# Performance work log

Hardware: AMD Instinct MI355X
Metric: run time of the kernel (lower is better)

The kernel has to match this reference:

```python
import jax, jax.numpy as jnp
import numpy as np

NUM_HEADS = 8


def _rope(t):
    # t: (b, h, L, hd). Interleaved-pair rotary embedding (rotary_embedding_torch style).
    hd = t.shape[-1]
    L = t.shape[-2]
    inv_freq = 1.0 / (10000.0 ** (jnp.arange(0, hd, 2, dtype=jnp.float32) / hd))  # (hd/2,)
    freqs = jnp.arange(L, dtype=jnp.float32)[:, None] * inv_freq[None, :]          # (L, hd/2)
    cos = jnp.repeat(jnp.cos(freqs), 2, axis=-1)  # (L, hd) interleaved
    sin = jnp.repeat(jnp.sin(freqs), 2, axis=-1)
    x2 = t.reshape(t.shape[:-1] + (hd // 2, 2))
    rot = jnp.stack((-x2[..., 1], x2[..., 0]), axis=-1).reshape(t.shape)
    return t * cos + rot * sin


def setup_inputs() -> dict:
    key = jax.random.key(0)
    ks = jax.random.split(key, 6)
    b, L, d = 2, 2048, 512
    s = 1.0 / np.sqrt(d)
    return {
        "x": jax.random.normal(ks[0], (b, L, d), jnp.float32),
        "prev": jax.random.normal(ks[1], (b, NUM_HEADS, L, L), jnp.float32) * 0.1,
        "Wq": jax.random.normal(ks[2], (d, d), jnp.float32) * s,
        "bq": jnp.zeros((d,), jnp.float32),
        "Wk": jax.random.normal(ks[3], (d, d), jnp.float32) * s,
        "bk": jnp.zeros((d,), jnp.float32),
        "Wv": jax.random.normal(ks[4], (d, d), jnp.float32) * s,
        "bv": jnp.zeros((d,), jnp.float32),
    }


def reference(x, prev, Wq, bq, Wk, bk, Wv, bv):
    b, L, d = x.shape
    h = NUM_HEADS
    hd = d // h

    def proj(W, bias):
        # torch nn.Linear: y = x @ W.T + b, then split heads -> (b, h, L, hd)
        return (x @ W.T + bias).reshape(b, L, h, hd).transpose(0, 2, 1, 3)

    q = _rope(proj(Wq, bq))
    k = _rope(proj(Wk, bk))
    v = proj(Wv, bv)

    score = jnp.einsum('bhqd,bhkd->bhqk', q, k) / np.float32(np.sqrt(hd))
    causal = jnp.tril(jnp.ones((L, L), dtype=bool))
    score = jnp.where(causal[None, None], score, jnp.float32(-1e9))
    score = score + prev  # RealFormer-style residual attention bias
    attn = jax.nn.softmax(score, axis=-1)
    o = jnp.einsum('bhqk,bhkd->bhqd', attn, v).transpose(0, 2, 1, 3).reshape(b, L, d)
    return o, score
```

## Files before the change

### kernel.cpp

```cpp
#include <hip/hip_runtime.h>
#include <hip/hip_bf16.h>
#include <math.h>

#define L_SEQ 2048
#define DM 512
#define NH 8
#define HD 64
#define ROPE_C 0.4152410118609203f

typedef __attribute__((ext_vector_type(8))) short bf16x8;
typedef __attribute__((ext_vector_type(8))) unsigned short u16x8;
typedef __attribute__((ext_vector_type(4))) float f32x4;

#define MFMA16(a, b, c) __builtin_amdgcn_mfma_f32_16x16x32_bf16((a), (b), (c), 0, 0, 0)

static __device__ __forceinline__ unsigned short f2bf(float f) {
    union { float f; unsigned int u; } c; c.f = f;
    unsigned int r = (c.u + 0x7fffu + ((c.u >> 16) & 1u)) >> 16;
    return (unsigned short)r;
}
static __device__ __forceinline__ float bf2f(unsigned short h) {
    union { unsigned int u; float f; } c; c.u = ((unsigned int)h) << 16;
    return c.f;
}

__global__ __launch_bounds__(256) void qkv_proj_mfma(
    const float* __restrict__ x,
    const float* __restrict__ Wq, const float* __restrict__ bq,
    const float* __restrict__ Wk, const float* __restrict__ bk,
    const float* __restrict__ Wv, const float* __restrict__ bv,
    unsigned short* __restrict__ Qh, unsigned short* __restrict__ Ql,
    unsigned short* __restrict__ Kh, unsigned short* __restrict__ Kl,
    unsigned short* __restrict__ Vb)
{
    const int z = blockIdx.z;
    const float* __restrict__ W    = (z == 0) ? Wq : (z == 1) ? Wk : Wv;
    const float* __restrict__ bias = (z == 0) ? bq : (z == 1) ? bk : bv;

    __shared__ __align__(16) unsigned short Xh[64 * 64];
    __shared__ __align__(16) unsigned short Xl[64 * 64];
    __shared__ __align__(16) unsigned short Wh[64 * 64];
    __shared__ __align__(16) unsigned short Wl[64 * 64];

    const int t = threadIdx.x;
    const int w = t >> 6, l = t & 63;
    const int lr = l & 15, lg = l >> 4;
    const int mbase = blockIdx.x * 64;
    const int nbase = blockIdx.y * 64;

    const int sr = t & 63;
    const int sc = (t >> 6) * 16;

    f32x4 acc[4];
    #pragma unroll
    for (int nb = 0; nb < 4; ++nb) acc[nb] = (f32x4){0.f, 0.f, 0.f, 0.f};

    for (int k0 = 0; k0 < DM; k0 += 64) {
        __syncthreads();
        {
            const int ch0 = (t >> 6) * 2, sw = sr & 7;
            const float* xs = &x[(size_t)(mbase + sr) * DM + k0 + sc];
            const float* ws = &W[(size_t)(nbase + sr) * DM + k0 + sc];
            float xv[16], wv[16];
            #pragma unroll
            for (int i = 0; i < 4; ++i) {
                float4 a = *(const float4*)(xs + 4 * i);
                xv[4 * i + 0] = a.x; xv[4 * i + 1] = a.y; xv[4 * i + 2] = a.z; xv[4 * i + 3] = a.w;
                float4 b = *(const float4*)(ws + 4 * i);
                wv[4 * i + 0] = b.x; wv[4 * i + 1] = b.y; wv[4 * i + 2] = b.z; wv[4 * i + 3] = b.w;
            }
            u16x8 xh0, xl0, xh1, xl1, wh0, wl0, wh1, wl1;
            #pragma unroll
            for (int i = 0; i < 8; ++i) {
                unsigned short h;
                h = f2bf(xv[i]);     xh0[i] = h; xl0[i] = f2bf(xv[i] - bf2f(h));
                h = f2bf(xv[i + 8]); xh1[i] = h; xl1[i] = f2bf(xv[i + 8] - bf2f(h));
                h = f2bf(wv[i]);     wh0[i] = h; wl0[i] = f2bf(wv[i] - bf2f(h));
                h = f2bf(wv[i + 8]); wh1[i] = h; wl1[i] = f2bf(wv[i + 8] - bf2f(h));
            }
            *(u16x8*)&Xh[sr * 64 + (((ch0    ) ^ sw) << 3)] = xh0;
            *(u16x8*)&Xh[sr * 64 + (((ch0 + 1) ^ sw) << 3)] = xh1;
            *(u16x8*)&Xl[sr * 64 + (((ch0    ) ^ sw) << 3)] = xl0;
            *(u16x8*)&Xl[sr * 64 + (((ch0 + 1) ^ sw) << 3)] = xl1;
            *(u16x8*)&Wh[sr * 64 + (((ch0    ) ^ sw) << 3)] = wh0;
            *(u16x8*)&Wh[sr * 64 + (((ch0 + 1) ^ sw) << 3)] = wh1;
            *(u16x8*)&Wl[sr * 64 + (((ch0    ) ^ sw) << 3)] = wl0;
            *(u16x8*)&Wl[sr * 64 + (((ch0 + 1) ^ sw) << 3)] = wl1;
        }
        __syncthreads();

        #pragma unroll
        for (int kc = 0; kc < 2; ++kc) {
            const int arow = w * 16 + lr;
            const int aofs = arow * 64 + (((4 * kc + lg) ^ (arow & 7)) << 3);
            bf16x8 ah = *(const bf16x8*)&Xh[aofs];
            bf16x8 al = *(const bf16x8*)&Xl[aofs];
            #pragma unroll
            for (int nb = 0; nb < 4; ++nb) {
                const int brow = nb * 16 + lr;
                const int bofs = brow * 64 + (((4 * kc + lg) ^ (brow & 7)) << 3);
                bf16x8 bh_ = *(const bf16x8*)&Wh[bofs];
                bf16x8 bl_ = *(const bf16x8*)&Wl[bofs];
                acc[nb] = MFMA16(ah, bl_, acc[nb]);
                acc[nb] = MFMA16(al, bh_, acc[nb]);
                acc[nb] = MFMA16(ah, bh_, acc[nb]);
            }
        }
    }

    #pragma unroll
    for (int nb = 0; nb < 4; ++nb) {
        const int n    = nbase + nb * 16 + lr;
        const int head = n >> 6;
        const int dim  = n & 63;
        const float bval = bias[n];
        const float invf = exp2f(-ROPE_C * (float)(dim >> 1));
        #pragma unroll
        for (int r = 0; r < 4; ++r) {
            const int mg    = mbase + w * 16 + lg * 4 + r;
            const int batch = mg >> 11;
            const int pos   = mg & 2047;
            float v = acc[nb][r] + bval;
            if (z < 2) {
                const float pv = __shfl_xor(v, 1);
                float s, c;
                sincosf((float)pos * invf, &s, &c);
                v = (dim & 1) ? fmaf(v, c, pv * s) : fmaf(v, c, -pv * s);
            }
            const size_t oidx = (((size_t)(batch * NH + head)) * L_SEQ + pos) * HD + dim;
            if (z == 2) {
                Vb[oidx] = f2bf(v);
            } else {
                const unsigned short h  = f2bf(v);
                const unsigned short lo = f2bf(v - bf2f(h));
                if (z == 0) { Qh[oidx] = h; Ql[oidx] = lo; }
                else        { Kh[oidx] = h; Kl[oidx] = lo; }
            }
        }
    }
}

__global__ __launch_bounds__(256) void attn_mfma(
    const unsigned short* __restrict__ Qh, const unsigned short* __restrict__ Ql,
    const unsigned short* __restrict__ Kh, const unsigned short* __restrict__ Kl,
    const unsigned short* __restrict__ Vb, const float* __restrict__ prev,
    float* __restrict__ out_o, float* __restrict__ out_score)
{
    __shared__ __align__(16) unsigned short Ksh[64 * 64];
    __shared__ __align__(16) unsigned short Ksl[64 * 64];
    __shared__ __align__(16) unsigned short Vt[64 * 64];
    __shared__ __align__(16) unsigned short Ps[4 * 16 * 64];

    const int g  = blockIdx.x;
    const int bh = g & 15;
    const int gq = g >> 4;
    const int qt = (gq < 16) ? 31 - gq : gq - 16;
    const int t  = threadIdx.x;
    const int w  = t >> 6, l = t & 63;
    const int lr = l & 15, lg = l >> 4;
    const int qbase = qt << 6;

    const size_t hbase = (size_t)bh * L_SEQ * HD;

    bf16x8 qhf[2], qlf[2];
    {
        const size_t qoff = hbase + (size_t)(qbase + w * 16 + lr) * HD + lg * 8;
        qhf[0] = *(const bf16x8*)&Qh[qoff];
        qhf[1] = *(const bf16x8*)&Qh[qoff + 32];
        qlf[0] = *(const bf16x8*)&Ql[qoff];
        qlf[1] = *(const bf16x8*)&Ql[qoff + 32];
    }

    f32x4 accO[4];
    #pragma unroll
    for (int db = 0; db < 4; ++db) accO[db] = (f32x4){0.f, 0.f, 0.f, 0.f};
    float m_i[4] = {-INFINITY, -INFINITY, -INFINITY, -INFINITY};
    float l_i[4] = {0.f, 0.f, 0.f, 0.f};

    for (int kt = 0; kt <= qt; ++kt) {
        const int kbase = kt << 6;
        __syncthreads();

        const size_t srow = ((size_t)bh * L_SEQ + (qbase + w * 16)) * L_SEQ + kbase;
        float pvv[4][4];
        #pragma unroll
        for (int kb = 0; kb < 4; ++kb)
            #pragma unroll
            for (int r = 0; r < 4; ++r)
                pvv[kb][r] = prev[srow + (size_t)(lg * 4 + r) * L_SEQ + kb * 16 + lr];

        {
            const int r = t & 63, c32 = t >> 6;
            const int ch0 = 2 * c32, sw = r & 7;
            const size_t koff = hbase + (size_t)(kbase + r) * HD + c32 * 16;
            u16x8 k0 = *(const u16x8*)&Kh[koff];
            u16x8 k1 = *(const u16x8*)&Kh[koff + 8];
            *(u16x8*)&Ksh[r * 64 + (((ch0    ) ^ sw) << 3)] = k0;
            *(u16x8*)&Ksh[r * 64 + (((ch0 + 1) ^ sw) << 3)] = k1;
            u16x8 k2 = *(const u16x8*)&Kl[koff];
            u16x8 k3 = *(const u16x8*)&Kl[koff + 8];
            *(u16x8*)&Ksl[r * 64 + (((ch0    ) ^ sw) << 3)] = k2;
            *(u16x8*)&Ksl[r * 64 + (((ch0 + 1) ^ sw) << 3)] = k3;

            const int vk = t & 63, vd0 = (t >> 6) * 16;
            const size_t voff = hbase + (size_t)(kbase + vk) * HD + vd0;
            u16x8 va = *(const u16x8*)&Vb[voff];
            u16x8 vb2 = *(const u16x8*)&Vb[voff + 8];
            #pragma unroll
            for (int e = 0; e < 8; ++e) {
                int d = vd0 + e;
                Vt[d * 64 + ((((vk >> 3) ^ (d & 7))) << 3) + (vk & 7)] = va[e];
                d = vd0 + 8 + e;
                Vt[d * 64 + ((((vk >> 3) ^ (d & 7))) << 3) + (vk & 7)] = vb2[e];
            }
        }
        __syncthreads();

        f32x4 s[4];
        #pragma unroll
        for (int kb = 0; kb < 4; ++kb) s[kb] = (f32x4){0.f, 0.f, 0.f, 0.f};
        #pragma unroll
        for (int kc = 0; kc < 2; ++kc) {
            #pragma unroll
            for (int kb = 0; kb < 4; ++kb) {
                const int brow = kb * 16 + lr;
                const int bofs = brow * 64 + (((4 * kc + lg) ^ (brow & 7)) << 3);
                bf16x8 bh_ = *(const bf16x8*)&Ksh[bofs];
                bf16x8 bl_ = *(const bf16x8*)&Ksl[bofs];
                s[kb] = MFMA16(qhf[kc], bl_, s[kb]);
                s[kb] = MFMA16(qlf[kc], bh_, s[kb]);
                s[kb] = MFMA16(qhf[kc], bh_, s[kb]);
            }
        }

        float vout[4][4];
        #pragma unroll
        for (int kb = 0; kb < 4; ++kb) {
            #pragma unroll
            for (int r = 0; r < 4; ++r) {
                const int kg = kbase + kb * 16 + lr;
                const int qg = qbase + w * 16 + lg * 4 + r;
                const float v = (kg <= qg) ? fmaf(s[kb][r], 0.125f, pvv[kb][r]) : -1e9f;
                vout[kb][r] = v;
                out_score[srow + (size_t)(lg * 4 + r) * L_SEQ + kb * 16 + lr] = v;
            }
        }

        #pragma unroll
        for (int r = 0; r < 4; ++r) {
            float mx = fmaxf(fmaxf(vout[0][r], vout[1][r]), fmaxf(vout[2][r], vout[3][r]));
            mx = fmaxf(mx, __shfl_xor(mx, 1));
            mx = fmaxf(mx, __shfl_xor(mx, 2));
            mx = fmaxf(mx, __shfl_xor(mx, 4));
            mx = fmaxf(mx, __shfl_xor(mx, 8));
            const float mnew = fmaxf(m_i[r], mx);
            const float sc = __expf(m_i[r] - mnew);
            float p[4], psum = 0.f;
            #pragma unroll
            for (int kb = 0; kb < 4; ++kb) { p[kb] = __expf(vout[kb][r] - mnew); psum += p[kb]; }
            psum += __shfl_xor(psum, 1);
            psum += __shfl_xor(psum, 2);
            psum += __shfl_xor(psum, 4);
            psum += __shfl_xor(psum, 8);
            l_i[r] = l_i[r] * sc + psum;
            m_i[r] = mnew;
            #pragma unroll
            for (int db = 0; db < 4; ++db) accO[db][r] *= sc;
            const int qloc = lg * 4 + r, swp = qloc & 7;
            #pragma unroll
            for (int kb = 0; kb < 4; ++kb) {
                const int kcol = kb * 16 + lr;
                Ps[w * 1024 + qloc * 64 + ((((kcol >> 3) ^ swp)) << 3) + (kcol & 7)] = f2bf(p[kb]);
            }
        }

        #pragma unroll
        for (int kc = 0; kc < 2; ++kc) {
            const int aofs = w * 1024 + lr * 64 + (((4 * kc + lg) ^ (lr & 7)) << 3);
            bf16x8 pa = *(const bf16x8*)&Ps[aofs];
            #pragma unroll
            for (int db = 0; db < 4; ++db) {
                const int vrow = db * 16 + lr;
                const int bofs = vrow * 64 + (((4 * kc + lg) ^ (vrow & 7)) << 3);
                bf16x8 vf = *(const bf16x8*)&Vt[bofs];
                accO[db] = MFMA16(pa, vf, accO[db]);
            }
        }
    }

    const int bb = bh >> 3, hh = bh & 7;
    #pragma unroll
    for (int r = 0; r < 4; ++r) {
        const int qg = qbase + w * 16 + lg * 4 + r;
        const float inv = 1.0f / l_i[r];
        #pragma unroll
        for (int db = 0; db < 4; ++db)
            out_o[((size_t)bb * L_SEQ + qg) * DM + hh * HD + db * 16 + lr] = accO[db][r] * inv;
    }

    const int endk = (qt + 1) << 6;
    if (endk < L_SEQ) {
        const float4 fv = make_float4(-1e9f, -1e9f, -1e9f, -1e9f);
        const int row = qbase + (t >> 2);
        const size_t rb = ((size_t)bh * L_SEQ + row) * L_SEQ;
        for (int c = endk + (t & 3) * 4; c < L_SEQ; c += 16)
            *(float4*)&out_score[rb + c] = fv;
    }
}

extern "C" void kernel_launch(void* const* d_in, const int* in_sizes, int n_in,
                              void* d_out, int out_size, void* d_ws, size_t ws_size,
                              hipStream_t stream)
{
    const float* x    = (const float*)d_in[0];
    const float* prev = (const float*)d_in[1];
    const float* Wq   = (const float*)d_in[2];
    const float* bq   = (const float*)d_in[3];
    const float* Wk   = (const float*)d_in[4];
    const float* bk   = (const float*)d_in[5];
    const float* Wv   = (const float*)d_in[6];
    const float* bv   = (const float*)d_in[7];

    float* out_o     = (float*)d_out;
    float* out_score = out_o + (size_t)2 * L_SEQ * DM;

    const size_t qkv_elems = (size_t)2 * NH * L_SEQ * HD;
    unsigned short* Qh = (unsigned short*)d_ws;
    unsigned short* Ql = Qh + qkv_elems;
    unsigned short* Kh = Ql + qkv_elems;
    unsigned short* Kl = Kh + qkv_elems;
    unsigned short* Vb = Kl + qkv_elems;

    qkv_proj_mfma<<<dim3(64, 8, 3), 256, 0, stream>>>(
        x, Wq, bq, Wk, bk, Wv, bv, Qh, Ql, Kh, Kl, Vb);

    attn_mfma<<<dim3(512), 256, 0, stream>>>(
        Qh, Ql, Kh, Kl, Vb, prev, out_o, out_score);
}
```

Before: 584.7 us.

## Pair short and long query tiles per block to balance causal work

Each block now handles two 32-row query tiles taken from opposite ends of the sequence, two waves per tile, instead of one 64-row tile. This balances per-block causal work across the grid. Waves whose tile has finished skip compute but still join the shared K/V loads and barriers. Shared K/V loads are now amortized over fewer query rows, and the masked-fill tail is reorganized per wave.

```diff
diff --git a/kernel.cpp b/kernel.cpp
--- a/kernel.cpp
+++ b/kernel.cpp
@@ -151,20 +151,24 @@
     __shared__ __align__(16) unsigned short Vt[64 * 64];
     __shared__ __align__(16) unsigned short Ps[4 * 16 * 64];
 
-    const int g  = blockIdx.x;
-    const int bh = g & 15;
-    const int gq = g >> 4;
-    const int qt = (gq < 16) ? 31 - gq : gq - 16;
-    const int t  = threadIdx.x;
-    const int w  = t >> 6, l = t & 63;
-    const int lr = l & 15, lg = l >> 4;
-    const int qbase = qt << 6;
+    const int g   = blockIdx.x;
+    const int bh  = g & 15;
+    const int qtA = g >> 4;
+    const int qtB = 63 - qtA;
+    const int t   = threadIdx.x;
+    const int w   = t >> 6, l = t & 63;
+    const int lr  = l & 15, lg = l >> 4;
+
+    const int myQt    = (w < 2) ? qtA : qtB;
+    const int myQbase = myQt * 32 + (w & 1) * 16;
+    const int myNkt   = myQt / 2 + 1;
+    const int sweep   = qtB / 2 + 1;
 
     const size_t hbase = (size_t)bh * L_SEQ * HD;
 
     bf16x8 qhf[2], qlf[2];
     {
-        const size_t qoff = hbase + (size_t)(qbase + w * 16 + lr) * HD + lg * 8;
+        const size_t qoff = hbase + (size_t)(myQbase + lr) * HD + lg * 8;
         qhf[0] = *(const bf16x8*)&Qh[qoff];
         qhf[1] = *(const bf16x8*)&Qh[qoff + 32];
         qlf[0] = *(const bf16x8*)&Ql[qoff];
@@ -177,17 +181,22 @@
     float m_i[4] = {-INFINITY, -INFINITY, -INFINITY, -INFINITY};
     float l_i[4] = {0.f, 0.f, 0.f, 0.f};
 
-    for (int kt = 0; kt <= qt; ++kt) {
+    const size_t srow0 = ((size_t)bh * L_SEQ + myQbase) * L_SEQ;
+
+    for (int kt = 0; kt < sweep; ++kt) {
         const int kbase = kt << 6;
+        const bool active = (kt < myNkt);
         __syncthreads();
 
-        const size_t srow = ((size_t)bh * L_SEQ + (qbase + w * 16)) * L_SEQ + kbase;
+        const size_t srow = srow0 + kbase;
         float pvv[4][4];
-        #pragma unroll
-        for (int kb = 0; kb < 4; ++kb)
-            #pragma unroll
-            for (int r = 0; r < 4; ++r)
-                pvv[kb][r] = prev[srow + (size_t)(lg * 4 + r) * L_SEQ + kb * 16 + lr];
+        if (active) {
+            #pragma unroll
+            for (int kb = 0; kb < 4; ++kb)
+                #pragma unroll
+                for (int r = 0; r < 4; ++r)
+                    pvv[kb][r] = prev[srow + (size_t)(lg * 4 + r) * L_SEQ + kb * 16 + lr];
+        }
 
         {
             const int r = t & 63, c32 = t >> 6;
@@ -204,7 +213,7 @@
 
             const int vk = t & 63, vd0 = (t >> 6) * 16;
             const size_t voff = hbase + (size_t)(kbase + vk) * HD + vd0;
-            u16x8 va = *(const u16x8*)&Vb[voff];
+            u16x8 va  = *(const u16x8*)&Vb[voff];
             u16x8 vb2 = *(const u16x8*)&Vb[voff + 8];
             #pragma unroll
             for (int e = 0; e < 8; ++e) {
@@ -216,74 +225,76 @@
         }
         __syncthreads();
 
-        f32x4 s[4];
-        #pragma unroll
-        for (int kb = 0; kb < 4; ++kb) s[kb] = (f32x4){0.f, 0.f, 0.f, 0.f};
-        #pragma unroll
-        for (int kc = 0; kc < 2; ++kc) {
+        if (active) {
+            f32x4 s[4];
+            #pragma unroll
+            for (int kb = 0; kb < 4; ++kb) s[kb] = (f32x4){0.f, 0.f, 0.f, 0.f};
+            #pragma unroll
+            for (int kc = 0; kc < 2; ++kc) {
+                #pragma unroll
+                for (int kb = 0; kb < 4; ++kb) {
+                    const int brow = kb * 16 + lr;
+                    const int bofs = brow * 64 + (((4 * kc + lg) ^ (brow & 7)) << 3);
+                    bf16x8 bh_ = *(const bf16x8*)&Ksh[bofs];
+                    bf16x8 bl_ = *(const bf16x8*)&Ksl[bofs];
+                    s[kb] = MFMA16(qhf[kc], bl_, s[kb]);
+                    s[kb] = MFMA16(qlf[kc], bh_, s[kb]);
+                    s[kb] = MFMA16(qhf[kc], bh_, s[kb]);
+                }
+            }
+
+            float vout[4][4];
             #pragma unroll
             for (int kb = 0; kb < 4; ++kb) {
-                const int brow = kb * 16 + lr;
-                const int bofs = brow * 64 + (((4 * kc + lg) ^ (brow & 7)) << 3);
-                bf16x8 bh_ = *(const bf16x8*)&Ksh[bofs];
-                bf16x8 bl_ = *(const bf16x8*)&Ksl[bofs];
-                s[kb] = MFMA16(qhf[kc], bl_, s[kb]);
-                s[kb] = MFMA16(qlf[kc], bh_, s[kb]);
-                s[kb] = MFMA16(qhf[kc], bh_, s[kb]);
-            }
-        }
-
-        float vout[4][4];
-        #pragma unroll
-        for (int kb = 0; kb < 4; ++kb) {
+                #pragma unroll
+                for (int r = 0; r < 4; ++r) {
+                    const int kg = kbase + kb * 16 + lr;
+                    const int qg = myQbase + lg * 4 + r;
+                    const float v = (kg <= qg) ? fmaf(s[kb][r], 0.125f, pvv[kb][r]) : -1e9f;
+                    vout[kb][r] = v;
+                    out_score[srow + (size_t)(lg * 4 + r) * L_SEQ + kb * 16 + lr] = v;
+                }
+            }
+
             #pragma unroll
             for (int r = 0; r < 4; ++r) {
-                const int kg = kbase + kb * 16 + lr;
-                const int qg = qbase + w * 16 + lg * 4 + r;
-                const float v = (kg <= qg) ? fmaf(s[kb][r], 0.125f, pvv[kb][r]) : -1e9f;
-                vout[kb][r] = v;
-                out_score[srow + (size_t)(lg * 4 + r) * L_SEQ + kb * 16 + lr] = v;
-            }
-        }
-
-        #pragma unroll
-        for (int r = 0; r < 4; ++r) {
-            float mx = fmaxf(fmaxf(vout[0][r], vout[1][r]), fmaxf(vout[2][r], vout[3][r]));
-            mx = fmaxf(mx, __shfl_xor(mx, 1));
-            mx = fmaxf(mx, __shfl_xor(mx, 2));
-            mx = fmaxf(mx, __shfl_xor(mx, 4));
-            mx = fmaxf(mx, __shfl_xor(mx, 8));
-            const float mnew = fmaxf(m_i[r], mx);
-            const float sc = __expf(m_i[r] - mnew);
-            float p[4], psum = 0.f;
-            #pragma unroll
-            for (int kb = 0; kb < 4; ++kb) { p[kb] = __expf(vout[kb][r] - mnew); psum += p[kb]; }
-            psum += __shfl_xor(psum, 1);
-            psum += __shfl_xor(psum, 2);
-            psum += __shfl_xor(psum, 4);
-            psum += __shfl_xor(psum, 8);
-            l_i[r] = l_i[r] * sc + psum;
-            m_i[r] = mnew;
-            #pragma unroll
-            for (int db = 0; db < 4; ++db) accO[db][r] *= sc;
-            const int qloc = lg * 4 + r, swp = qloc & 7;
-            #pragma unroll
-            for (int kb = 0; kb < 4; ++kb) {
-                const int kcol = kb * 16 + lr;
-                Ps[w * 1024 + qloc * 64 + ((((kcol >> 3) ^ swp)) << 3) + (kcol & 7)] = f2bf(p[kb]);
-            }
-        }
-
-        #pragma unroll
-        for (int kc = 0; kc < 2; ++kc) {
-            const int aofs = w * 1024 + lr * 64 + (((4 * kc + lg) ^ (lr & 7)) << 3);
-            bf16x8 pa = *(const bf16x8*)&Ps[aofs];
-            #pragma unroll
-            for (int db = 0; db < 4; ++db) {
-                const int vrow = db * 16 + lr;
-                const int bofs = vrow * 64 + (((4 * kc + lg) ^ (vrow & 7)) << 3);
-                bf16x8 vf = *(const bf16x8*)&Vt[bofs];
-                accO[db] = MFMA16(pa, vf, accO[db]);
+                float mx = fmaxf(fmaxf(vout[0][r], vout[1][r]), fmaxf(vout[2][r], vout[3][r]));
+                mx = fmaxf(mx, __shfl_xor(mx, 1));
+                mx = fmaxf(mx, __shfl_xor(mx, 2));
+                mx = fmaxf(mx, __shfl_xor(mx, 4));
+                mx = fmaxf(mx, __shfl_xor(mx, 8));
+                const float mnew = fmaxf(m_i[r], mx);
+                const float sc = __expf(m_i[r] - mnew);
+                float p[4], psum = 0.f;
+                #pragma unroll
+                for (int kb = 0; kb < 4; ++kb) { p[kb] = __expf(vout[kb][r] - mnew); psum += p[kb]; }
+                psum += __shfl_xor(psum, 1);
+                psum += __shfl_xor(psum, 2);
+                psum += __shfl_xor(psum, 4);
+                psum += __shfl_xor(psum, 8);
+                l_i[r] = l_i[r] * sc + psum;
+                m_i[r] = mnew;
+                #pragma unroll
+                for (int db = 0; db < 4; ++db) accO[db][r] *= sc;
+                const int qloc = lg * 4 + r, swp = qloc & 7;
+                #pragma unroll
+                for (int kb = 0; kb < 4; ++kb) {
+                    const int kcol = kb * 16 + lr;
+                    Ps[w * 1024 + qloc * 64 + ((((kcol >> 3) ^ swp)) << 3) + (kcol & 7)] = f2bf(p[kb]);
+                }
+            }
+
+            #pragma unroll
+            for (int kc = 0; kc < 2; ++kc) {
+                const int aofs = w * 1024 + lr * 64 + (((4 * kc + lg) ^ (lr & 7)) << 3);
+                bf16x8 pa = *(const bf16x8*)&Ps[aofs];
+                #pragma unroll
+                for (int db = 0; db < 4; ++db) {
+                    const int vrow = db * 16 + lr;
+                    const int bofs = vrow * 64 + (((4 * kc + lg) ^ (vrow & 7)) << 3);
+                    bf16x8 vf = *(const bf16x8*)&Vt[bofs];
+                    accO[db] = MFMA16(pa, vf, accO[db]);
+                }
             }
         }
     }
@@ -291,19 +302,19 @@
     const int bb = bh >> 3, hh = bh & 7;
     #pragma unroll
     for (int r = 0; r < 4; ++r) {
-        const int qg = qbase + w * 16 + lg * 4 + r;
+        const int qg = myQbase + lg * 4 + r;
         const float inv = 1.0f / l_i[r];
         #pragma unroll
         for (int db = 0; db < 4; ++db)
             out_o[((size_t)bb * L_SEQ + qg) * DM + hh * HD + db * 16 + lr] = accO[db][r] * inv;
     }
 
-    const int endk = (qt + 1) << 6;
-    if (endk < L_SEQ) {
+    {
+        const int c0 = myNkt << 6;
+        const int row = myQbase + lr;
+        const size_t rb = ((size_t)bh * L_SEQ + row) * L_SEQ;
         const float4 fv = make_float4(-1e9f, -1e9f, -1e9f, -1e9f);
-        const int row = qbase + (t >> 2);
-        const size_t rb = ((size_t)bh * L_SEQ + row) * L_SEQ;
-        for (int c = endk + (t & 3) * 4; c < L_SEQ; c += 16)
+        for (int c = c0 + lg * 4; c < L_SEQ; c += 16)
             *(float4*)&out_score[rb + c] = fv;
     }
 }
```

Result: slower. 620.0 us (+6.0%).
